# Kernel tuning notes

Hardware: AMD Instinct MI355X
Metric: run time of the kernel (lower is better)

The kernel has to match this reference:

```python
import jax, jax.numpy as jnp
import numpy as np

PAD = 1  # PAD_token; embedding rows at PAD are zero (padding_idx)


def setup_inputs() -> dict:
    V, D, HOPS = 50000, 128, 3
    B, Lc, Mc = 16, 256, 8
    Lk, Mk = 512, 8
    key = jax.random.key(0)
    kC, kK, kc, kk = jax.random.split(key, 4)
    # one table per hop (C_0..C_{HOPS-1}, K_0..K_{HOPS-1}), init N(0, 0.1)
    C = 0.1 * jax.random.normal(kC, (HOPS, V, D), dtype=jnp.float32)
    K = 0.1 * jax.random.normal(kK, (HOPS, V, D), dtype=jnp.float32)
    C = C.at[:, PAD].set(0.0)
    K = K.at[:, PAD].set(0.0)
    conv_seqs = jax.random.randint(kc, (B, Lc, Mc), 0, V)
    kb_arr = jax.random.randint(kk, (B, Lk, Mk), 0, V)  # dense, PAD-padded ragged KB
    return {"conv_seqs": conv_seqs, "kb_arr": kb_arr, "C": C, "K": K}


def reference(conv_seqs, kb_arr, C, K):
    B, Lc, _ = conv_seqs.shape
    HOPS, _, D = C.shape
    conv_feature = jnp.zeros((B, Lc, D), dtype=C.dtype)
    for hop in range(HOPS):
        # embedding-bag: gather + sum over span tokens
        cf = jnp.sum(C[hop][conv_seqs], axis=2)  # [B, Lc, D]
        kf = jnp.sum(K[hop][kb_arr], axis=2)     # [B, Lk, D]
        att = jnp.einsum('bld,bkd->blk', cf, kf)  # [B, Lc, Lk]
        p = jax.nn.softmax(att, axis=-1)
        conv_feature = jnp.einsum('blk,bkd->bld', p, kf) + conv_feature
    return conv_feature.transpose(1, 0, 2)  # [Lc, B, D]
```

## Files before the change

kernel.cpp:

```cpp
#include <hip/hip_runtime.h>

#define V_    50000
#define D_    128
#define HOPS_ 3
#define B_    16
#define LC_   256
#define MC_   8
#define LK_   512
#define MK_   8

typedef __bf16  bf16x8  __attribute__((ext_vector_type(8)));
typedef unsigned short ushort8 __attribute__((ext_vector_type(8)));
typedef unsigned short ushort4v __attribute__((ext_vector_type(4)));
typedef float   floatx4 __attribute__((ext_vector_type(4)));

__device__ inline unsigned short f2bf(float f) {
    union { float f; unsigned u; } x; x.f = f;
    unsigned r = x.u + 0x7FFFu + ((x.u >> 16) & 1u);
    return (unsigned short)(r >> 16);
}

__device__ inline floatx4 mfma_bf16(ushort8 a, ushort8 b, floatx4 c) {
    return __builtin_amdgcn_mfma_f32_16x16x32_bf16(
        __builtin_bit_cast(bf16x8, a), __builtin_bit_cast(bf16x8, b), c, 0, 0, 0);
}

__global__ __launch_bounds__(256, 7) void gather_kernel(
    const int* __restrict__ conv_seqs, const int* __restrict__ kb_arr,
    const float* __restrict__ Ct, const float* __restrict__ Kt,
    unsigned short* __restrict__ kf, unsigned short* __restrict__ cf)
{
    const int tid  = threadIdx.x;
    const int r    = tid >> 3;
    const int s    = tid & 7;
    const int lane = tid & 63;
    const int bx   = blockIdx.x;

    constexpr int KBLK = HOPS_ * B_ * (LK_ / 32);

    const int*   idxp;
    const float* table;
    unsigned short* dst;

    if (bx < KBLK) {
        int hop  = bx / (B_ * 16);
        int rem  = bx % (B_ * 16);
        int b    = rem >> 4;
        int row0 = (rem & 15) * 32;
        idxp  = kb_arr + (size_t)(b * LK_ + row0 + r) * MK_;
        table = Kt + (size_t)hop * V_ * D_;
        dst   = kf + (((size_t)(hop * B_ + b) * LK_) + row0 + r) * D_;
    } else {
        int id   = bx - KBLK;
        int hop  = id / (B_ * 8);
        int rem  = id % (B_ * 8);
        int b    = rem >> 3;
        int row0 = (rem & 7) * 32;
        idxp  = conv_seqs + (size_t)(b * LC_ + row0 + r) * MC_;
        table = Ct + (size_t)hop * V_ * D_;
        dst   = cf + (((size_t)(hop * B_ + b) * LC_) + row0 + r) * D_;
    }

    const int myidx = idxp[s];
    int idxs[8];
    #pragma unroll
    for (int m = 0; m < 8; ++m)
        idxs[m] = __shfl(myidx, (lane & 56) + m);

    float4 acc[4];
    #pragma unroll
    for (int j = 0; j < 4; ++j) acc[j] = make_float4(0.f, 0.f, 0.f, 0.f);

    #pragma unroll
    for (int m = 0; m < 8; ++m) {
        const float* rowp = table + (size_t)idxs[m] * D_;
        #pragma unroll
        for (int j = 0; j < 4; ++j) {
            float4 v = *(const float4*)(rowp + j * 32 + s * 4);
            acc[j].x += v.x; acc[j].y += v.y; acc[j].z += v.z; acc[j].w += v.w;
        }
    }

    #pragma unroll
    for (int j = 0; j < 4; ++j) {
        ushort4v o;
        o[0] = f2bf(acc[j].x); o[1] = f2bf(acc[j].y);
        o[2] = f2bf(acc[j].z); o[3] = f2bf(acc[j].w);
        *(ushort4v*)(dst + j * 32 + s * 4) = o;
    }
}

__global__ __launch_bounds__(256) void transpose_kernel(
    const unsigned short* __restrict__ kf, unsigned short* __restrict__ kfT,
    float4* __restrict__ out4)
{
    __shared__ unsigned short tile[64][72];

    const int tid = threadIdx.x;
    const int bx  = blockIdx.x;

    if (bx >= 768) {
        out4[(size_t)(bx - 768) * 256 + tid] = make_float4(0.f, 0.f, 0.f, 0.f);
        return;
    }

    const int g  = bx >> 4;
    const int dt = (bx & 15) >> 3;
    const int kt = bx & 7;
    const int k0 = kt * 64, d0 = dt * 64;

    const int r = tid >> 2;
    const int c = tid & 3;

    const unsigned short* src = kf + ((size_t)g * 512 + k0 + r) * 128 + d0 + c * 16;
    ushort8 a = *(const ushort8*)(src);
    ushort8 b = *(const ushort8*)(src + 8);
    *(ushort8*)&tile[r][c * 16]     = a;
    *(ushort8*)&tile[r][c * 16 + 8] = b;
    __syncthreads();

    unsigned short* dstp = kfT + ((size_t)g * 128 + d0 + r) * 512 + k0 + c * 16;
    ushort8 o0, o1;
    #pragma unroll
    for (int i = 0; i < 8; ++i) o0[i] = tile[c * 16 + i][r];
    #pragma unroll
    for (int i = 0; i < 8; ++i) o1[i] = tile[c * 16 + 8 + i][r];
    *(ushort8*)(dstp)     = o0;
    *(ushort8*)(dstp + 8) = o1;
}

__global__ __launch_bounds__(512) void attn_kernel(
    const unsigned short* __restrict__ kf, const unsigned short* __restrict__ kfT,
    const unsigned short* __restrict__ cf, float* __restrict__ out)
{
    constexpr int AS = 516;
    __shared__ float att_s[16][AS];
    __shared__ float rowinv_s[16];

    const int tid  = threadIdx.x;
    const int wave = tid >> 6;
    const int lane = tid & 63;
    const int quad = lane >> 4;
    const int l16  = lane & 15;

    const int gl  = blockIdx.x & 7;
    const int s_  = blockIdx.x >> 3;
    const int lt  = s_ / 6;
    const int gh  = s_ % 6;
    const int g   = gh * 8 + gl;
    const int b   = g & 15;
    const int l0  = lt * 16;

    const unsigned short* cf_h  = cf  + (((size_t)g) * 256 + l0) * 128;
    const unsigned short* kf_h  = kf  + ((size_t)g) * 512 * 128;
    const unsigned short* kfT_h = kfT + ((size_t)g) * 128 * 512;

    ushort8 afrag[4];
    #pragma unroll
    for (int ks = 0; ks < 4; ++ks)
        afrag[ks] = *(const ushort8*)(cf_h + l16 * 128 + ks * 32 + quad * 8);

    #pragma unroll
    for (int t = 0; t < 4; ++t) {
        const int nt = wave * 4 + t;
        floatx4 acc = {0.f, 0.f, 0.f, 0.f};
        #pragma unroll
        for (int ks = 0; ks < 4; ++ks) {
            ushort8 bfrag = *(const ushort8*)(kf_h + (nt * 16 + l16) * 128 + ks * 32 + quad * 8);
            acc = mfma_bf16(afrag[ks], bfrag, acc);
        }
        #pragma unroll
        for (int rr = 0; rr < 4; ++rr)
            att_s[quad * 4 + rr][nt * 16 + l16] = acc[rr];
    }
    __syncthreads();

    #pragma unroll
    for (int rr = 0; rr < 2; ++rr) {
        const int row = wave * 2 + rr;
        float v[8];
        float mx = -1e30f;
        #pragma unroll
        for (int j = 0; j < 8; ++j) {
            v[j] = att_s[row][lane + j * 64];
            mx = fmaxf(mx, v[j]);
        }
        #pragma unroll
        for (int off = 32; off; off >>= 1) mx = fmaxf(mx, __shfl_xor(mx, off));
        float sum = 0.f;
        #pragma unroll
        for (int j = 0; j < 8; ++j) {
            float e = __expf(v[j] - mx);
            att_s[row][lane + j * 64] = e;
            sum += e;
        }
        #pragma unroll
        for (int off = 32; off; off >>= 1) sum += __shfl_xor(sum, off);
        if (lane == 0) rowinv_s[row] = 1.0f / sum;
    }
    __syncthreads();

    floatx4 pacc = {0.f, 0.f, 0.f, 0.f};
    #pragma unroll
    for (int ks = 0; ks < 16; ++ks) {
        const float* prow = &att_s[l16][ks * 32 + quad * 8];
        float4 p0 = *(const float4*)(prow);
        float4 p1 = *(const float4*)(prow + 4);
        ushort8 pa;
        pa[0] = f2bf(p0.x); pa[1] = f2bf(p0.y); pa[2] = f2bf(p0.z); pa[3] = f2bf(p0.w);
        pa[4] = f2bf(p1.x); pa[5] = f2bf(p1.y); pa[6] = f2bf(p1.z); pa[7] = f2bf(p1.w);
        ushort8 bfrag = *(const ushort8*)(kfT_h + (size_t)(wave * 16 + l16) * 512 + ks * 32 + quad * 8);
        pacc = mfma_bf16(pa, bfrag, pacc);
    }

    const int d = wave * 16 + l16;
    #pragma unroll
    for (int rr = 0; rr < 4; ++rr)
        atomicAdd(&out[(((size_t)(l0 + quad * 4 + rr)) * 16 + b) * 128 + d],
                  pacc[rr] * rowinv_s[quad * 4 + rr]);
}

extern "C" void kernel_launch(void* const* d_in, const int* in_sizes, int n_in,
                              void* d_out, int out_size, void* d_ws, size_t ws_size,
                              hipStream_t stream) {
    (void)in_sizes; (void)n_in; (void)out_size; (void)ws_size;
    const int*   conv_seqs = (const int*)d_in[0];
    const int*   kb_arr    = (const int*)d_in[1];
    const float* C         = (const float*)d_in[2];
    const float* K         = (const float*)d_in[3];

    unsigned short* kf  = (unsigned short*)d_ws;
    unsigned short* kfT = kf  + (size_t)HOPS_ * B_ * LK_ * D_;
    unsigned short* cf  = kfT + (size_t)HOPS_ * B_ * LK_ * D_;
    float* out = (float*)d_out;

    hipLaunchKernelGGL(gather_kernel, dim3(1152), dim3(256), 0, stream,
                       conv_seqs, kb_arr, C, K, kf, cf);
    hipLaunchKernelGGL(transpose_kernel, dim3(1280), dim3(256), 0, stream,
                       kf, kfT, (float4*)out);
    hipLaunchKernelGGL(attn_kernel, dim3(768), dim3(512), 0, stream,
                       kf, kfT, cf, out);
}
```

Baseline: 194.2 us.

## Fuse K transpose and output zeroing into gather kernel; precompute bf16 probabilities

```diff
diff --git a/kernel.cpp b/kernel.cpp
--- a/kernel.cpp
+++ b/kernel.cpp
@@ -28,37 +28,54 @@
 __global__ __launch_bounds__(256, 7) void gather_kernel(
     const int* __restrict__ conv_seqs, const int* __restrict__ kb_arr,
     const float* __restrict__ Ct, const float* __restrict__ Kt,
-    unsigned short* __restrict__ kf, unsigned short* __restrict__ cf)
+    unsigned short* __restrict__ kf, unsigned short* __restrict__ kfT,
+    unsigned short* __restrict__ cf, float4* __restrict__ out4)
 {
+    __shared__ unsigned short tile[32][132];
+
     const int tid  = threadIdx.x;
+    const int bx   = blockIdx.x;
+
+    constexpr int KBLK = HOPS_ * B_ * (LK_ / 32);
+    constexpr int CBLK = HOPS_ * B_ * (LC_ / 32);
+
+    if (bx >= KBLK + CBLK) {
+        out4[(size_t)(bx - (KBLK + CBLK)) * 256 + tid] =
+            make_float4(0.f, 0.f, 0.f, 0.f);
+        return;
+    }
+
     const int r    = tid >> 3;
     const int s    = tid & 7;
     const int lane = tid & 63;
-    const int bx   = blockIdx.x;
-
-    constexpr int KBLK = HOPS_ * B_ * (LK_ / 32);
 
     const int*   idxp;
     const float* table;
     unsigned short* dst;
+    bool do_transpose;
+    int g, row0;
 
     if (bx < KBLK) {
         int hop  = bx / (B_ * 16);
         int rem  = bx % (B_ * 16);
         int b    = rem >> 4;
-        int row0 = (rem & 15) * 32;
+        row0 = (rem & 15) * 32;
+        g    = hop * B_ + b;
         idxp  = kb_arr + (size_t)(b * LK_ + row0 + r) * MK_;
         table = Kt + (size_t)hop * V_ * D_;
-        dst   = kf + (((size_t)(hop * B_ + b) * LK_) + row0 + r) * D_;
+        dst   = kf + ((size_t)g * LK_ + row0 + r) * D_;
+        do_transpose = true;
     } else {
         int id   = bx - KBLK;
         int hop  = id / (B_ * 8);
         int rem  = id % (B_ * 8);
         int b    = rem >> 3;
-        int row0 = (rem & 7) * 32;
+        row0 = (rem & 7) * 32;
+        g    = hop * B_ + b;
         idxp  = conv_seqs + (size_t)(b * LC_ + row0 + r) * MC_;
         table = Ct + (size_t)hop * V_ * D_;
-        dst   = cf + (((size_t)(hop * B_ + b) * LC_) + row0 + r) * D_;
+        dst   = cf + ((size_t)g * LC_ + row0 + r) * D_;
+        do_transpose = false;
     }
 
     const int myidx = idxp[s];
@@ -81,52 +98,31 @@
         }
     }
 
+    ushort4v o[4];
     #pragma unroll
     for (int j = 0; j < 4; ++j) {
-        ushort4v o;
-        o[0] = f2bf(acc[j].x); o[1] = f2bf(acc[j].y);
-        o[2] = f2bf(acc[j].z); o[3] = f2bf(acc[j].w);
-        *(ushort4v*)(dst + j * 32 + s * 4) = o;
-    }
-}
-
-__global__ __launch_bounds__(256) void transpose_kernel(
-    const unsigned short* __restrict__ kf, unsigned short* __restrict__ kfT,
-    float4* __restrict__ out4)
-{
-    __shared__ unsigned short tile[64][72];
-
-    const int tid = threadIdx.x;
-    const int bx  = blockIdx.x;
-
-    if (bx >= 768) {
-        out4[(size_t)(bx - 768) * 256 + tid] = make_float4(0.f, 0.f, 0.f, 0.f);
-        return;
-    }
-
-    const int g  = bx >> 4;
-    const int dt = (bx & 15) >> 3;
-    const int kt = bx & 7;
-    const int k0 = kt * 64, d0 = dt * 64;
-
-    const int r = tid >> 2;
-    const int c = tid & 3;
-
-    const unsigned short* src = kf + ((size_t)g * 512 + k0 + r) * 128 + d0 + c * 16;
-    ushort8 a = *(const ushort8*)(src);
-    ushort8 b = *(const ushort8*)(src + 8);
-    *(ushort8*)&tile[r][c * 16]     = a;
-    *(ushort8*)&tile[r][c * 16 + 8] = b;
-    __syncthreads();
-
-    unsigned short* dstp = kfT + ((size_t)g * 128 + d0 + r) * 512 + k0 + c * 16;
-    ushort8 o0, o1;
-    #pragma unroll
-    for (int i = 0; i < 8; ++i) o0[i] = tile[c * 16 + i][r];
-    #pragma unroll
-    for (int i = 0; i < 8; ++i) o1[i] = tile[c * 16 + 8 + i][r];
-    *(ushort8*)(dstp)     = o0;
-    *(ushort8*)(dstp + 8) = o1;
+        o[j][0] = f2bf(acc[j].x); o[j][1] = f2bf(acc[j].y);
+        o[j][2] = f2bf(acc[j].z); o[j][3] = f2bf(acc[j].w);
+        *(ushort4v*)(dst + j * 32 + s * 4) = o[j];
+    }
+
+    if (do_transpose) {
+        #pragma unroll
+        for (int j = 0; j < 4; ++j)
+            *(ushort4v*)&tile[r][j * 32 + s * 4] = o[j];
+        __syncthreads();
+        const int d    = tid >> 1;
+        const int half = tid & 1;
+        unsigned short* tdst =
+            kfT + ((size_t)g * D_ + d) * LK_ + row0 + half * 16;
+        ushort8 a, b;
+        #pragma unroll
+        for (int i = 0; i < 8; ++i) a[i] = tile[half * 16 + i][d];
+        #pragma unroll
+        for (int i = 0; i < 8; ++i) b[i] = tile[half * 16 + 8 + i][d];
+        *(ushort8*)(tdst)     = a;
+        *(ushort8*)(tdst + 8) = b;
+    }
 }
 
 __global__ __launch_bounds__(512) void attn_kernel(
@@ -134,7 +130,9 @@
     const unsigned short* __restrict__ cf, float* __restrict__ out)
 {
     constexpr int AS = 516;
+    constexpr int PS = 520;
     __shared__ float att_s[16][AS];
+    __shared__ unsigned short p_s[16][PS];
     __shared__ float rowinv_s[16];
 
     const int tid  = threadIdx.x;
@@ -191,7 +189,7 @@
         #pragma unroll
         for (int j = 0; j < 8; ++j) {
             float e = __expf(v[j] - mx);
-            att_s[row][lane + j * 64] = e;
+            p_s[row][lane + j * 64] = f2bf(e);
             sum += e;
         }
         #pragma unroll
@@ -203,12 +201,7 @@
     floatx4 pacc = {0.f, 0.f, 0.f, 0.f};
     #pragma unroll
     for (int ks = 0; ks < 16; ++ks) {
-        const float* prow = &att_s[l16][ks * 32 + quad * 8];
-        float4 p0 = *(const float4*)(prow);
-        float4 p1 = *(const float4*)(prow + 4);
-        ushort8 pa;
-        pa[0] = f2bf(p0.x); pa[1] = f2bf(p0.y); pa[2] = f2bf(p0.z); pa[3] = f2bf(p0.w);
-        pa[4] = f2bf(p1.x); pa[5] = f2bf(p1.y); pa[6] = f2bf(p1.z); pa[7] = f2bf(p1.w);
+        ushort8 pa    = *(const ushort8*)&p_s[l16][ks * 32 + quad * 8];
         ushort8 bfrag = *(const ushort8*)(kfT_h + (size_t)(wave * 16 + l16) * 512 + ks * 32 + quad * 8);
         pacc = mfma_bf16(pa, bfrag, pacc);
     }
@@ -234,10 +227,8 @@
     unsigned short* cf  = kfT + (size_t)HOPS_ * B_ * LK_ * D_;
     float* out = (float*)d_out;
 
-    hipLaunchKernelGGL(gather_kernel, dim3(1152), dim3(256), 0, stream,
-                       conv_seqs, kb_arr, C, K, kf, cf);
-    hipLaunchKernelGGL(transpose_kernel, dim3(1280), dim3(256), 0, stream,
-                       kf, kfT, (float4*)out);
+    hipLaunchKernelGGL(gather_kernel, dim3(1664), dim3(256), 0, stream,
+                       conv_seqs, kb_arr, C, K, kf, kfT, cf, (float4*)out);
     hipLaunchKernelGGL(attn_kernel, dim3(768), dim3(512), 0, stream,
                        kf, kfT, cf, out);
 }
```

New measurement: 190.5 us. About the same (-1.9%).
